# Performance work log

Hardware: AMD Instinct MI355X
Metric: run time of the kernel (lower is better)

## Reference

```python
import jax, jax.numpy as jnp
import numpy as np

L, DIN, D, NL = 16384, 256, 768, 8
EPS = 1e-5


def _ln(x, g, b):
    mu = jnp.mean(x, axis=-1, keepdims=True)
    var = jnp.mean(jnp.square(x - mu), axis=-1, keepdims=True)
    return (x - mu) * jax.lax.rsqrt(var + EPS) * g + b


def setup_inputs() -> dict:
    key = jax.random.key(0)
    ks = iter(jax.random.split(key, 24))
    nrm = lambda shape, s=0.02: jax.random.normal(next(ks), shape, jnp.float32) * s
    return {
        "node_features": jax.random.normal(next(ks), (L, DIN), jnp.float32),
        "W_proj": nrm((DIN, D)), "b_proj": jnp.zeros((D,), jnp.float32),
        "ln_s_g": jnp.ones((NL, D), jnp.float32), "ln_s_b": jnp.zeros((NL, D), jnp.float32),
        "W_in": nrm((NL, D, D)), "b_in": jnp.zeros((NL, D), jnp.float32),
        "W_gate": nrm((NL, D, D)), "b_gate": jnp.zeros((NL, D), jnp.float32),
        "W_out": nrm((NL, D, D)), "b_out": jnp.zeros((NL, D), jnp.float32),
        "decay_logit": nrm((NL, D), 0.5),
        "ln_f_g": jnp.ones((NL, D), jnp.float32), "ln_f_b": jnp.zeros((NL, D), jnp.float32),
        "W_ff1": nrm((NL, D, 2 * D)), "b_ff1": jnp.zeros((NL, 2 * D), jnp.float32),
        "W_ff2": nrm((NL, 2 * D, D)), "b_ff2": jnp.zeros((NL, D), jnp.float32),
        "ln_o_g": jnp.ones((D,), jnp.float32), "ln_o_b": jnp.zeros((D,), jnp.float32),
    }


def reference(node_features, W_proj, b_proj, ln_s_g, ln_s_b, W_in, b_in,
              W_gate, b_gate, W_out, b_out, decay_logit, ln_f_g, ln_f_b,
              W_ff1, b_ff1, W_ff2, b_ff2, ln_o_g, ln_o_b):
    x = node_features @ W_proj + b_proj  # [L, D]
    for l in range(NL):
        h = _ln(x, ln_s_g[l], ln_s_b[l])
        u = h @ W_in[l] + b_in[l]                      # [L, D]
        gate = jax.nn.sigmoid(h @ W_gate[l] + b_gate[l])
        decay = jax.nn.sigmoid(decay_logit[l])         # [D]

        def step(state, u_t):
            state = decay * state + u_t
            return state, state

        _, states = jax.lax.scan(step, jnp.zeros((D,), x.dtype), u)  # [L, D]
        x = x + (states * gate) @ W_out[l] + b_out[l]
        hf = _ln(x, ln_f_g[l], ln_f_b[l])
        x = x + jax.nn.silu(hf @ W_ff1[l] + b_ff1[l]) @ W_ff2[l] + b_ff2[l]
    return _ln(x, ln_o_g, ln_o_b)
```

## Files before the change

### kernel.cpp

```cpp
#include <hip/hip_runtime.h>
#include <hip/hip_bf16.h>
#include <math.h>
#include <string.h>

#define L_TOK 16384
#define D_INP 256
#define D_MOD 768
#define D_FF  1536
#define N_LAYER 8
#define S_T 64
#define S_G 256
#define EPSV 1e-5f

typedef short bf16x8 __attribute__((ext_vector_type(8)));
typedef float f32x4 __attribute__((ext_vector_type(4)));
typedef __hip_bfloat16 bf16;
typedef unsigned int u32;
typedef unsigned short u16;

__device__ __forceinline__ float fsigmoid(float z) { return 1.0f / (1.0f + __expf(-z)); }

__device__ __forceinline__ u16 f2bf(float f) {
  __hip_bfloat16 h = __float2bfloat16(f);
  u16 r; memcpy(&r, &h, 2); return r;
}
__device__ __forceinline__ float bf2f(u16 v) {
  u32 x = ((u32)v) << 16; float f; memcpy(&f, &x, 4); return f;
}

__device__ __forceinline__ void glds16(const short* g, short* l) {
  __builtin_amdgcn_global_load_lds(
      (const __attribute__((address_space(1))) unsigned int*)(g),
      (__attribute__((address_space(3))) unsigned int*)(l), 16, 0, 0);
}

__device__ __forceinline__ bf16x8 dsr128(const char* base, int imm) {
  bf16x8 r;
  const __attribute__((address_space(3))) char* p =
      (const __attribute__((address_space(3))) char*)base;
  asm volatile("ds_read_b128 %0, %1 offset:%c2" : "=v"(r) : "v"(p), "i"(imm));
  return r;
}

__global__ void k_f32_to_bf16v(const float4* __restrict__ src, ushort4* __restrict__ dst, int n4) {
  int i = blockIdx.x * blockDim.x + threadIdx.x;
  if (i < n4) {
    float4 v = src[i];
    ushort4 o; o.x = f2bf(v.x); o.y = f2bf(v.y); o.z = f2bf(v.z); o.w = f2bf(v.w);
    dst[i] = o;
  }
}

template<bool FOLD>
__global__ void k_transpose_fold(const float* __restrict__ src, bf16* __restrict__ dst,
                                 int R, int C, size_t sstride, size_t dstride,
                                 const float* __restrict__ gv, const float* __restrict__ bv,
                                 float* __restrict__ wacc, float* __restrict__ bacc,
                                 int vstride) {
  __shared__ float tile[32][33];
  int z = blockIdx.z;
  const float* s = src + (size_t)z * sstride;
  bf16* d = dst + (size_t)z * dstride;
  int r0 = blockIdx.y * 32, c0 = blockIdx.x * 32;
  int tx = threadIdx.x, ty = threadIdx.y;
#pragma unroll
  for (int i = ty; i < 32; i += 8)
    tile[i][tx] = s[(size_t)(r0 + i) * C + (c0 + tx)];
  __syncthreads();
  float gk = 1.0f;
  if (FOLD) gk = gv[(size_t)z * R + r0 + tx];
#pragma unroll
  for (int i = ty; i < 32; i += 8) {
    float val = tile[tx][i];
    if (FOLD) val *= gk;
    d[(size_t)(c0 + i) * R + (r0 + tx)] = __float2bfloat16(val);
  }
  if (FOLD && ty == 0) {
    const float* gz = gv + (size_t)z * R + r0;
    const float* bz = bv + (size_t)z * R + r0;
    float s1 = 0.f, s2 = 0.f;
#pragma unroll 8
    for (int j = 0; j < 32; j++) {
      float wv = tile[j][tx];
      s1 += gz[j] * wv;
      s2 += bz[j] * wv;
    }
    atomicAdd(&wacc[(size_t)z * vstride + c0 + tx], s1);
    atomicAdd(&bacc[(size_t)z * vstride + c0 + tx], s2);
  }
}

template<int MODE, bool LNFOLD, bool STATS>
__global__ __launch_bounds__(256, 4) void k_gemm128(
    const short* __restrict__ A, const short* __restrict__ Bt,
    const float* __restrict__ bias, const float* __restrict__ bias2,
    const float* __restrict__ wvec, const float* __restrict__ bvec,
    const float* __restrict__ stats_in, float* __restrict__ stats_out,
    u16* __restrict__ res, u16* __restrict__ outp, u16* __restrict__ outp2,
    int N, int K, int ncol)
{
  __shared__ short As[3][128 * 32];
  __shared__ short Bs[3][128 * 32];
  __shared__ float s_mu[128], s_rv[128];
  const int tid = threadIdx.x;
  const int lane = tid & 63, w = tid >> 6;
  const int wr = w >> 1, wc = w & 1;
  const int l16 = lane & 15, qd = lane >> 4;

  const int b = blockIdx.x;
  const int xcd = b & 7, t = b >> 3;
  const int m0 = (xcd * 16 + t / ncol) * 128;
  const int n0 = (t % ncol) * 128;

  const int sr = lane >> 2, sc = lane & 3;
  const int ar = w * 32 + sr;
  const int acx = sc ^ ((ar >> 1) & 3);
  const short* ag0 = A  + (size_t)(m0 + ar) * K + acx * 8;
  const short* ag1 = ag0 + (size_t)16 * K;
  const short* bg0 = Bt + (size_t)(n0 + ar) * K + acx * 8;
  const short* bg1 = bg0 + (size_t)16 * K;

  auto stg = [&](int bi, int k0) {
    short* a0 = &As[bi][w * 1024];
    glds16(ag0 + k0, a0); glds16(ag1 + k0, a0 + 512);
    short* b0 = &Bs[bi][w * 1024];
    glds16(bg0 + k0, b0); glds16(bg1 + k0, b0 + 512);
  };

  const int fo = (qd ^ ((l16 >> 1) & 3)) * 8 + l16 * 32;

  float sv = 0.f, sq = 0.f;
  if (LNFOLD && tid < 128) {
    sv = stats_in[2 * (m0 + tid)];
    sq = stats_in[2 * (m0 + tid) + 1];
  }

  const int NT = K >> 5;
  stg(0, 0);
  stg(1, 32);

  if (LNFOLD && tid < 128) {
    float mu  = sv * (1.0f / (float)D_MOD);
    float var = sq * (1.0f / (float)D_MOD) - mu * mu;
    s_mu[tid] = mu;
    s_rv[tid] = 1.0f / sqrtf(var + EPSV);
  }

  f32x4 acc[4][4];
#pragma unroll
  for (int i = 0; i < 4; i++)
#pragma unroll
    for (int j = 0; j < 4; j++) acc[i][j] = (f32x4){0.f, 0.f, 0.f, 0.f};

  asm volatile("s_waitcnt vmcnt(4)" ::: "memory");
  __builtin_amdgcn_s_barrier();

  int rd = 0;
  for (int t2 = 0; t2 < NT; ++t2) {
    const char* ab = (const char*)&As[rd][wr * 2048 + fo];
    const char* bb = (const char*)&Bs[rd][wc * 2048 + fo];
    bf16x8 af0 = dsr128(ab, 0),    af1 = dsr128(ab, 1024);
    bf16x8 af2 = dsr128(ab, 2048), af3 = dsr128(ab, 3072);
    bf16x8 bf0 = dsr128(bb, 0),    bf1 = dsr128(bb, 1024);
    bf16x8 bf2 = dsr128(bb, 2048), bf3 = dsr128(bb, 3072);
    if (t2 + 2 < NT) {
      int st = (rd == 0) ? 2 : rd - 1;
      stg(st, (t2 + 2) * 32);
    }
    asm volatile("s_waitcnt lgkmcnt(0)" ::: "memory");
    __builtin_amdgcn_sched_barrier(0);
    bf16x8 af[4] = {af0, af1, af2, af3};
    bf16x8 bfr[4] = {bf0, bf1, bf2, bf3};
#pragma unroll
    for (int rt = 0; rt < 4; rt++)
#pragma unroll
      for (int ct = 0; ct < 4; ct++)
        acc[rt][ct] = __builtin_amdgcn_mfma_f32_16x16x32_bf16(af[rt], bfr[ct], acc[rt][ct], 0, 0, 0);
    if (t2 + 2 < NT) asm volatile("s_waitcnt vmcnt(4)" ::: "memory");
    else             asm volatile("s_waitcnt vmcnt(0)" ::: "memory");
    __builtin_amdgcn_s_barrier();
    rd = (rd == 2) ? 0 : rd + 1;
  }

  const float* bb = bias;
  u16* op = outp;
  int nofs = 0, Nout = N;
  bool sig = false;
  if (MODE == 4) {
    Nout = N >> 1;
    if (n0 >= Nout) { bb = bias2; op = outp2; nofs = Nout; sig = true; }
  }
  const int gmb = m0 + wr * 64 + qd * 4;
  const int gnb = n0 + wc * 64 + l16;
  float bc[4], wv4[4], bv4[4];
#pragma unroll
  for (int ct = 0; ct < 4; ct++) {
    int gn = gnb + ct * 16;
    bc[ct] = bb[gn - nofs];
    if (LNFOLD) { wv4[ct] = wvec[gn]; bv4[ct] = bvec[gn]; }
  }
#pragma unroll
  for (int rt = 0; rt < 4; rt++) {
#pragma unroll
    for (int r = 0; r < 4; r++) {
      const int gm = gmb + rt * 16 + r;
      float mu = 0.f, rv = 0.f;
      if (LNFOLD) { mu = s_mu[gm - m0]; rv = s_rv[gm - m0]; }
      float ps = 0.f, ps2 = 0.f;
#pragma unroll
      for (int ct = 0; ct < 4; ct++) {
        int gn = gnb + ct * 16;
        float vv = acc[rt][ct][r];
        if (LNFOLD) vv = rv * vv - rv * mu * wv4[ct] + bv4[ct] + bc[ct];
        else        vv += bc[ct];
        if (MODE == 2) vv = vv * fsigmoid(vv);
        if (MODE == 4 && sig) vv = fsigmoid(vv);
        size_t oidx = (size_t)gm * Nout + (gn - nofs);
        if (MODE == 3) vv += bf2f(res[oidx]);
        u16 rb = f2bf(vv);
        op[oidx] = rb;
        if (STATS) { float fv = bf2f(rb); ps += fv; ps2 += fv * fv; }
      }
      if (STATS) {
#pragma unroll
        for (int o = 1; o < 16; o <<= 1) {
          ps  += __shfl_xor(ps, o, 64);
          ps2 += __shfl_xor(ps2, o, 64);
        }
        if (l16 == 0) {
          atomicAdd(&stats_out[2 * gm], ps);
          atomicAdd(&stats_out[2 * gm + 1], ps2);
        }
      }
    }
  }
}

__global__ void k_scan_a(const bf16* __restrict__ u, const float* __restrict__ dl,
                         float* __restrict__ clast) {
  int t = threadIdx.x;
  int g = blockIdx.x;
  int d0 = t * 4;
  float dec[4], s[4] = {0.f, 0.f, 0.f, 0.f};
#pragma unroll
  for (int c = 0; c < 4; c++) dec[c] = fsigmoid(dl[d0 + c]);
  const ushort4* up = (const ushort4*)(u + (size_t)g * S_T * D_MOD) + t;
  for (int tt = 0; tt < S_T; tt++) {
    ushort4 uv = up[(size_t)tt * 192];
    s[0] = fmaf(dec[0], s[0], bf2f(uv.x));
    s[1] = fmaf(dec[1], s[1], bf2f(uv.y));
    s[2] = fmaf(dec[2], s[2], bf2f(uv.z));
    s[3] = fmaf(dec[3], s[3], bf2f(uv.w));
  }
#pragma unroll
  for (int c = 0; c < 4; c++) clast[(size_t)g * D_MOD + d0 + c] = s[c];
}

__global__ void k_scan_b(const float* __restrict__ clast, const float* __restrict__ dl,
                         float* __restrict__ carry) {
  int d = threadIdx.x;
  float decay = fsigmoid(dl[d]);
  float aT = decay;
#pragma unroll
  for (int i = 0; i < 6; i++) aT *= aT;
  float c = 0.f;
  for (int g = 0; g < S_G; g++) {
    carry[(size_t)g * D_MOD + d] = c;
    c = fmaf(aT, c, clast[(size_t)g * D_MOD + d]);
  }
}

__global__ void k_scan_c(const bf16* __restrict__ u, const float* __restrict__ dl,
                         const float* __restrict__ carry, bf16* __restrict__ gate_s) {
  int t = threadIdx.x;
  int g = blockIdx.x;
  int d0 = t * 4;
  float dec[4], s[4];
#pragma unroll
  for (int c = 0; c < 4; c++) {
    dec[c] = fsigmoid(dl[d0 + c]);
    s[c] = carry[(size_t)g * D_MOD + d0 + c];
  }
  const ushort4* up = (const ushort4*)(u + (size_t)g * S_T * D_MOD) + t;
  ushort4* gp = (ushort4*)(gate_s + (size_t)g * S_T * D_MOD) + t;
  for (int tt = 0; tt < S_T; tt++) {
    ushort4 uv = up[(size_t)tt * 192];
    ushort4 gv = gp[(size_t)tt * 192];
    s[0] = fmaf(dec[0], s[0], bf2f(uv.x));
    s[1] = fmaf(dec[1], s[1], bf2f(uv.y));
    s[2] = fmaf(dec[2], s[2], bf2f(uv.z));
    s[3] = fmaf(dec[3], s[3], bf2f(uv.w));
    ushort4 ov;
    ov.x = f2bf(s[0] * bf2f(gv.x));
    ov.y = f2bf(s[1] * bf2f(gv.y));
    ov.z = f2bf(s[2] * bf2f(gv.z));
    ov.w = f2bf(s[3] * bf2f(gv.w));
    gp[(size_t)tt * 192] = ov;
  }
}

__global__ __launch_bounds__(256) void k_ln_final(const u16* __restrict__ x,
    const float* __restrict__ stats, const float* __restrict__ g,
    const float* __restrict__ b, float* __restrict__ outp) {
  int wv = threadIdx.x >> 6, lane = threadIdx.x & 63;
  int row = blockIdx.x * 4 + wv;
  float sv = stats[2 * row], sq = stats[2 * row + 1];
  float mu = sv * (1.0f / (float)D_MOD);
  float var = sq * (1.0f / (float)D_MOD) - mu * mu;
  float rv = 1.0f / sqrtf(var + EPSV);
  const ushort4* xr = (const ushort4*)(x + (size_t)row * D_MOD);
  const float4* g4 = (const float4*)g;
  const float4* b4 = (const float4*)b;
  float4* o4 = (float4*)(outp + (size_t)row * D_MOD);
#pragma unroll
  for (int j = 0; j < 3; j++) {
    int f = j * 64 + lane;
    ushort4 xv = xr[f];
    float4 gg = g4[f], bb = b4[f], ov;
    ov.x = (bf2f(xv.x) - mu) * rv * gg.x + bb.x;
    ov.y = (bf2f(xv.y) - mu) * rv * gg.y + bb.y;
    ov.z = (bf2f(xv.z) - mu) * rv * gg.z + bb.z;
    ov.w = (bf2f(xv.w) - mu) * rv * gg.w + bb.w;
    o4[f] = ov;
  }
}

extern "C" void kernel_launch(void* const* d_in, const int* in_sizes, int n_in,
                              void* d_out, int out_size, void* d_ws, size_t ws_size,
                              hipStream_t stream) {
  const float* nf     = (const float*)d_in[0];
  const float* W_proj = (const float*)d_in[1];
  const float* b_proj = (const float*)d_in[2];
  const float* ln_s_g = (const float*)d_in[3];
  const float* ln_s_b = (const float*)d_in[4];
  const float* W_in   = (const float*)d_in[5];
  const float* b_in   = (const float*)d_in[6];
  const float* W_gate = (const float*)d_in[7];
  const float* b_gate = (const float*)d_in[8];
  const float* W_out  = (const float*)d_in[9];
  const float* b_out  = (const float*)d_in[10];
  const float* dlogit = (const float*)d_in[11];
  const float* ln_f_g = (const float*)d_in[12];
  const float* ln_f_b = (const float*)d_in[13];
  const float* W_ff1  = (const float*)d_in[14];
  const float* b_ff1  = (const float*)d_in[15];
  const float* W_ff2  = (const float*)d_in[16];
  const float* b_ff2  = (const float*)d_in[17];
  const float* ln_o_g = (const float*)d_in[18];
  const float* ln_o_b = (const float*)d_in[19];
  (void)in_sizes; (void)n_in;

  char* ws = (char*)d_ws;
  size_t off = 0;
  auto alloc = [&](size_t bytes) -> char* {
    char* p = ws + off;
    off = (off + bytes + 255) & ~(size_t)255;
    return p;
  };
  const bool big = ws_size >= (160ull << 20);
  const size_t wmul = big ? N_LAYER : 1;

  u16*   x     = (u16*)alloc(2ull * L_TOK * D_MOD);
  char*  ug    = alloc(2ull * L_TOK * D_FF);
  u16*   u     = (u16*)ug;
  u16*   gate  = (u16*)(ug + 2ull * L_TOK * D_MOD);
  u16*   tb    = (u16*)ug;
  u16*   nfb   = (u16*)ug;
  bf16*  WprojT= (bf16*)alloc(2ull * D_INP * D_MOD);
  bf16*  WigT  = (bf16*)alloc(2ull * wmul * (2 * D_MOD) * D_MOD);
  bf16*  WoT   = (bf16*)alloc(2ull * wmul * D_MOD * D_MOD);
  bf16*  Wff1T = (bf16*)alloc(2ull * wmul * D_MOD * D_FF);
  bf16*  Wff2T = (bf16*)alloc(2ull * wmul * D_FF * D_MOD);
  float* clast = (float*)alloc(sizeof(float) * (size_t)S_G * D_MOD);
  float* carry = (float*)alloc(sizeof(float) * (size_t)S_G * D_MOD);
  char*  zbase = alloc(0);
  float* stats = (float*)alloc(sizeof(float) * 17ull * L_TOK * 2);
  float* wvig  = (float*)alloc(sizeof(float) * N_LAYER * 2 * D_MOD);
  float* bvig  = (float*)alloc(sizeof(float) * N_LAYER * 2 * D_MOD);
  float* wvf1  = (float*)alloc(sizeof(float) * N_LAYER * D_FF);
  float* bvf1  = (float*)alloc(sizeof(float) * N_LAYER * D_FF);
  size_t zbytes = (size_t)((char*)ws + off - zbase);
  hipMemsetAsync(zbase, 0, zbytes, stream);

  const size_t DD = (size_t)D_MOD * D_MOD, DF = (size_t)D_MOD * D_FF;
  auto statslot = [&](int s) { return stats + (size_t)s * L_TOK * 2; };
  dim3 tb32(32, 8);
  k_f32_to_bf16v<<<(L_TOK * D_INP / 4 + 255) / 256, 256, 0, stream>>>(
      (const float4*)nf, (ushort4*)nfb, L_TOK * D_INP / 4);
  k_transpose_fold<false><<<dim3(D_MOD / 32, D_INP / 32, 1), tb32, 0, stream>>>(
      W_proj, WprojT, D_INP, D_MOD, 0, 0, nullptr, nullptr, nullptr, nullptr, 0);
  if (big) {
    k_transpose_fold<true><<<dim3(D_MOD / 32, D_MOD / 32, N_LAYER), tb32, 0, stream>>>(
        W_in,   WigT,      D_MOD, D_MOD, DD, 2 * DD, ln_s_g, ln_s_b, wvig,       bvig,       2 * D_MOD);
    k_transpose_fold<true><<<dim3(D_MOD / 32, D_MOD / 32, N_LAYER), tb32, 0, stream>>>(
        W_gate, WigT + DD, D_MOD, D_MOD, DD, 2 * DD, ln_s_g, ln_s_b, wvig + D_MOD, bvig + D_MOD, 2 * D_MOD);
    k_transpose_fold<false><<<dim3(D_MOD / 32, D_MOD / 32, N_LAYER), tb32, 0, stream>>>(
        W_out,  WoT,       D_MOD, D_MOD, DD, DD, nullptr, nullptr, nullptr, nullptr, 0);
    k_transpose_fold<true><<<dim3(D_FF / 32,  D_MOD / 32, N_LAYER), tb32, 0, stream>>>(
        W_ff1,  Wff1T,     D_MOD, D_FF,  DF, DF, ln_f_g, ln_f_b, wvf1, bvf1, D_FF);
    k_transpose_fold<false><<<dim3(D_MOD / 32, D_FF / 32,  N_LAYER), tb32, 0, stream>>>(
        W_ff2,  Wff2T,     D_FF,  D_MOD, DF, DF, nullptr, nullptr, nullptr, nullptr, 0);
  }

  k_gemm128<0, false, true><<<128 * 6, 256, 0, stream>>>(
      (const short*)nfb, (const short*)WprojT, b_proj, nullptr, nullptr, nullptr,
      nullptr, statslot(0), nullptr, x, nullptr, D_MOD, D_INP, 6);

  for (int l = 0; l < N_LAYER; l++) {
    const bf16 *wigT, *woT, *wf1T, *wf2T;
    if (big) {
      wigT = WigT  + (size_t)l * 2 * DD;
      woT  = WoT   + (size_t)l * DD;
      wf1T = Wff1T + (size_t)l * DF;
      wf2T = Wff2T + (size_t)l * DF;
    } else {
      k_transpose_fold<true><<<dim3(D_MOD / 32, D_MOD / 32, 1), tb32, 0, stream>>>(
          W_in + (size_t)l * DD, WigT, D_MOD, D_MOD, 0, 0,
          ln_s_g + l * D_MOD, ln_s_b + l * D_MOD, wvig + (size_t)l * 2 * D_MOD, bvig + (size_t)l * 2 * D_MOD, 0);
      k_transpose_fold<true><<<dim3(D_MOD / 32, D_MOD / 32, 1), tb32, 0, stream>>>(
          W_gate + (size_t)l * DD, WigT + DD, D_MOD, D_MOD, 0, 0,
          ln_s_g + l * D_MOD, ln_s_b + l * D_MOD, wvig + (size_t)l * 2 * D_MOD + D_MOD, bvig + (size_t)l * 2 * D_MOD + D_MOD, 0);
      k_transpose_fold<false><<<dim3(D_MOD / 32, D_MOD / 32, 1), tb32, 0, stream>>>(
          W_out + (size_t)l * DD, WoT, D_MOD, D_MOD, 0, 0, nullptr, nullptr, nullptr, nullptr, 0);
      k_transpose_fold<true><<<dim3(D_FF / 32, D_MOD / 32, 1), tb32, 0, stream>>>(
          W_ff1 + (size_t)l * DF, Wff1T, D_MOD, D_FF, 0, 0,
          ln_f_g + l * D_MOD, ln_f_b + l * D_MOD, wvf1 + (size_t)l * D_FF, bvf1 + (size_t)l * D_FF, 0);
      k_transpose_fold<false><<<dim3(D_MOD / 32, D_FF / 32, 1), tb32, 0, stream>>>(
          W_ff2 + (size_t)l * DF, Wff2T, D_FF, D_MOD, 0, 0, nullptr, nullptr, nullptr, nullptr, 0);
      wigT = WigT; woT = WoT; wf1T = Wff1T; wf2T = Wff2T;
    }

    k_gemm128<4, true, false><<<128 * 12, 256, 0, stream>>>(
        (const short*)x, (const short*)wigT, b_in + l * D_MOD, b_gate + l * D_MOD,
        wvig + (size_t)l * 2 * D_MOD, bvig + (size_t)l * 2 * D_MOD,
        statslot(2 * l), nullptr, nullptr, u, gate, 2 * D_MOD, D_MOD, 12);
    k_scan_a<<<S_G, 192, 0, stream>>>((const bf16*)u, dlogit + l * D_MOD, clast);
    k_scan_b<<<1, D_MOD, 0, stream>>>(clast, dlogit + l * D_MOD, carry);
    k_scan_c<<<S_G, 192, 0, stream>>>((const bf16*)u, dlogit + l * D_MOD, carry, (bf16*)gate);
    k_gemm128<3, false, true><<<128 * 6, 256, 0, stream>>>(
        (const short*)gate, (const short*)woT, b_out + l * D_MOD, nullptr, nullptr, nullptr,
        nullptr, statslot(2 * l + 1), x, x, nullptr, D_MOD, D_MOD, 6);
    k_gemm128<2, true, false><<<128 * 12, 256, 0, stream>>>(
        (const short*)x, (const short*)wf1T, b_ff1 + l * D_FF, nullptr,
        wvf1 + (size_t)l * D_FF, bvf1 + (size_t)l * D_FF,
        statslot(2 * l + 1), nullptr, nullptr, tb, nullptr, D_FF, D_MOD, 12);
    k_gemm128<3, false, true><<<128 * 6, 256, 0, stream>>>(
        (const short*)tb, (const short*)wf2T, b_ff2 + l * D_MOD, nullptr, nullptr, nullptr,
        nullptr, statslot(2 * l + 2), x, x, nullptr, D_MOD, D_FF, 6);
  }

  k_ln_final<<<L_TOK / 4, 256, 0, stream>>>(x, statslot(2 * N_LAYER), ln_o_g, ln_o_b, (float*)d_out);
}
```

Before: 2.305 ms.

## Interleave LDS reads with MFMAs and fold carry scan into scan_c

The GEMM inner loop now issues the next global stage first, then reads the B and A fragments from LDS. It waits on lgkmcnt incrementally so each row of MFMAs starts as soon as its A fragment arrives, overlapping LDS latency with matrix math. The single-block k_scan_b kernel is removed: each k_scan_c block recomputes its own carry by serially combining all preceding chunk tails. This saves a launch and a serial 256-step kernel per layer, at the cost of redundant, quadratic-in-chunks reads of clast.

```diff
diff --git a/kernel.cpp b/kernel.cpp
--- a/kernel.cpp
+++ b/kernel.cpp
@@ -157,25 +157,41 @@
 
   int rd = 0;
   for (int t2 = 0; t2 < NT; ++t2) {
-    const char* ab = (const char*)&As[rd][wr * 2048 + fo];
-    const char* bb = (const char*)&Bs[rd][wc * 2048 + fo];
-    bf16x8 af0 = dsr128(ab, 0),    af1 = dsr128(ab, 1024);
-    bf16x8 af2 = dsr128(ab, 2048), af3 = dsr128(ab, 3072);
-    bf16x8 bf0 = dsr128(bb, 0),    bf1 = dsr128(bb, 1024);
-    bf16x8 bf2 = dsr128(bb, 2048), bf3 = dsr128(bb, 3072);
     if (t2 + 2 < NT) {
       int st = (rd == 0) ? 2 : rd - 1;
       stg(st, (t2 + 2) * 32);
     }
+    const char* ab = (const char*)&As[rd][wr * 2048 + fo];
+    const char* bb2 = (const char*)&Bs[rd][wc * 2048 + fo];
+    bf16x8 bf0 = dsr128(bb2, 0),    bf1 = dsr128(bb2, 1024);
+    bf16x8 bf2 = dsr128(bb2, 2048), bf3 = dsr128(bb2, 3072);
+    bf16x8 af0 = dsr128(ab, 0),     af1 = dsr128(ab, 1024);
+    bf16x8 af2 = dsr128(ab, 2048),  af3 = dsr128(ab, 3072);
+
+    asm volatile("s_waitcnt lgkmcnt(3)" ::: "memory");
+    __builtin_amdgcn_sched_barrier(0);
+    acc[0][0] = __builtin_amdgcn_mfma_f32_16x16x32_bf16(af0, bf0, acc[0][0], 0, 0, 0);
+    acc[0][1] = __builtin_amdgcn_mfma_f32_16x16x32_bf16(af0, bf1, acc[0][1], 0, 0, 0);
+    acc[0][2] = __builtin_amdgcn_mfma_f32_16x16x32_bf16(af0, bf2, acc[0][2], 0, 0, 0);
+    acc[0][3] = __builtin_amdgcn_mfma_f32_16x16x32_bf16(af0, bf3, acc[0][3], 0, 0, 0);
+    asm volatile("s_waitcnt lgkmcnt(2)" ::: "memory");
+    __builtin_amdgcn_sched_barrier(0);
+    acc[1][0] = __builtin_amdgcn_mfma_f32_16x16x32_bf16(af1, bf0, acc[1][0], 0, 0, 0);
+    acc[1][1] = __builtin_amdgcn_mfma_f32_16x16x32_bf16(af1, bf1, acc[1][1], 0, 0, 0);
+    acc[1][2] = __builtin_amdgcn_mfma_f32_16x16x32_bf16(af1, bf2, acc[1][2], 0, 0, 0);
+    acc[1][3] = __builtin_amdgcn_mfma_f32_16x16x32_bf16(af1, bf3, acc[1][3], 0, 0, 0);
+    asm volatile("s_waitcnt lgkmcnt(1)" ::: "memory");
+    __builtin_amdgcn_sched_barrier(0);
+    acc[2][0] = __builtin_amdgcn_mfma_f32_16x16x32_bf16(af2, bf0, acc[2][0], 0, 0, 0);
+    acc[2][1] = __builtin_amdgcn_mfma_f32_16x16x32_bf16(af2, bf1, acc[2][1], 0, 0, 0);
+    acc[2][2] = __builtin_amdgcn_mfma_f32_16x16x32_bf16(af2, bf2, acc[2][2], 0, 0, 0);
+    acc[2][3] = __builtin_amdgcn_mfma_f32_16x16x32_bf16(af2, bf3, acc[2][3], 0, 0, 0);
     asm volatile("s_waitcnt lgkmcnt(0)" ::: "memory");
     __builtin_amdgcn_sched_barrier(0);
-    bf16x8 af[4] = {af0, af1, af2, af3};
-    bf16x8 bfr[4] = {bf0, bf1, bf2, bf3};
-#pragma unroll
-    for (int rt = 0; rt < 4; rt++)
-#pragma unroll
-      for (int ct = 0; ct < 4; ct++)
-        acc[rt][ct] = __builtin_amdgcn_mfma_f32_16x16x32_bf16(af[rt], bfr[ct], acc[rt][ct], 0, 0, 0);
+    acc[3][0] = __builtin_amdgcn_mfma_f32_16x16x32_bf16(af3, bf0, acc[3][0], 0, 0, 0);
+    acc[3][1] = __builtin_amdgcn_mfma_f32_16x16x32_bf16(af3, bf1, acc[3][1], 0, 0, 0);
+    acc[3][2] = __builtin_amdgcn_mfma_f32_16x16x32_bf16(af3, bf2, acc[3][2], 0, 0, 0);
+    acc[3][3] = __builtin_amdgcn_mfma_f32_16x16x32_bf16(af3, bf3, acc[3][3], 0, 0, 0);
     if (t2 + 2 < NT) asm volatile("s_waitcnt vmcnt(4)" ::: "memory");
     else             asm volatile("s_waitcnt vmcnt(0)" ::: "memory");
     __builtin_amdgcn_s_barrier();
@@ -256,30 +272,28 @@
   for (int c = 0; c < 4; c++) clast[(size_t)g * D_MOD + d0 + c] = s[c];
 }
 
-__global__ void k_scan_b(const float* __restrict__ clast, const float* __restrict__ dl,
-                         float* __restrict__ carry) {
-  int d = threadIdx.x;
-  float decay = fsigmoid(dl[d]);
-  float aT = decay;
-#pragma unroll
-  for (int i = 0; i < 6; i++) aT *= aT;
-  float c = 0.f;
-  for (int g = 0; g < S_G; g++) {
-    carry[(size_t)g * D_MOD + d] = c;
-    c = fmaf(aT, c, clast[(size_t)g * D_MOD + d]);
-  }
-}
-
 __global__ void k_scan_c(const bf16* __restrict__ u, const float* __restrict__ dl,
-                         const float* __restrict__ carry, bf16* __restrict__ gate_s) {
+                         const float* __restrict__ clast, bf16* __restrict__ gate_s) {
   int t = threadIdx.x;
   int g = blockIdx.x;
   int d0 = t * 4;
-  float dec[4], s[4];
+  float dec[4], aT[4], s[4];
 #pragma unroll
   for (int c = 0; c < 4; c++) {
     dec[c] = fsigmoid(dl[d0 + c]);
-    s[c] = carry[(size_t)g * D_MOD + d0 + c];
+    float a = dec[c];
+#pragma unroll
+    for (int i = 0; i < 6; i++) a *= a;
+    aT[c] = a;
+    s[c] = 0.f;
+  }
+  const float4* cl = (const float4*)clast + t;
+  for (int j = 0; j < g; j++) {
+    float4 cv = cl[(size_t)j * 192];
+    s[0] = fmaf(aT[0], s[0], cv.x);
+    s[1] = fmaf(aT[1], s[1], cv.y);
+    s[2] = fmaf(aT[2], s[2], cv.z);
+    s[3] = fmaf(aT[3], s[3], cv.w);
   }
   const ushort4* up = (const ushort4*)(u + (size_t)g * S_T * D_MOD) + t;
   ushort4* gp = (ushort4*)(gate_s + (size_t)g * S_T * D_MOD) + t;
@@ -372,7 +386,6 @@
   bf16*  Wff1T = (bf16*)alloc(2ull * wmul * D_MOD * D_FF);
   bf16*  Wff2T = (bf16*)alloc(2ull * wmul * D_FF * D_MOD);
   float* clast = (float*)alloc(sizeof(float) * (size_t)S_G * D_MOD);
-  float* carry = (float*)alloc(sizeof(float) * (size_t)S_G * D_MOD);
   char*  zbase = alloc(0);
   float* stats = (float*)alloc(sizeof(float) * 17ull * L_TOK * 2);
   float* wvig  = (float*)alloc(sizeof(float) * N_LAYER * 2 * D_MOD);
@@ -435,8 +448,7 @@
         wvig + (size_t)l * 2 * D_MOD, bvig + (size_t)l * 2 * D_MOD,
         statslot(2 * l), nullptr, nullptr, u, gate, 2 * D_MOD, D_MOD, 12);
     k_scan_a<<<S_G, 192, 0, stream>>>((const bf16*)u, dlogit + l * D_MOD, clast);
-    k_scan_b<<<1, D_MOD, 0, stream>>>(clast, dlogit + l * D_MOD, carry);
-    k_scan_c<<<S_G, 192, 0, stream>>>((const bf16*)u, dlogit + l * D_MOD, carry, (bf16*)gate);
+    k_scan_c<<<S_G, 192, 0, stream>>>((const bf16*)u, dlogit + l * D_MOD, clast, (bf16*)gate);
     k_gemm128<3, false, true><<<128 * 6, 256, 0, stream>>>(
         (const short*)gate, (const short*)woT, b_out + l * D_MOD, nullptr, nullptr, nullptr,
         nullptr, statslot(2 * l + 1), x, x, nullptr, D_MOD, D_MOD, 6);
```

Result: slower. 2.631 ms (+14.1%).
